# Performance work log

Hardware: AMD Instinct MI355X
Metric: run time of the kernel (lower is better)

The kernel has to match this reference:

```python
import jax, jax.numpy as jnp
import numpy as np
from jax import lax

NUM_CLASSES = 10
NUM_ITER = 3
CAP_DIM = 8       # primary capsule dim
OUT_CAP_DIM = 16  # digit capsule dim
NUM_MAP = 32      # 256 / 8
NUM_PRIM = 144    # 12*12


def squash(x, axis=-1):
    s2 = jnp.sum(x * x, axis=axis, keepdims=True)
    return (s2 / (1.0 + s2)) * x / jnp.sqrt(s2 + 1e-8)


def conv2d(x, w, b):
    y = lax.conv_general_dilated(x, w, (1, 1), 'VALID',
                                 dimension_numbers=('NCHW', 'OIHW', 'NCHW'))
    return y + b[None, :, None, None]


def setup_inputs() -> dict:
    key = jax.random.key(0)
    ks = jax.random.split(key, 13)
    B = 128
    return {
        'imgs': jax.random.uniform(ks[0], (B, 1, 28, 28), dtype=jnp.float32),
        'conv1_w': jax.random.normal(ks[1], (256, 1, 9, 9), jnp.float32) * 0.05,
        'conv1_b': jnp.zeros((256,), jnp.float32),
        'conv2_w': jax.random.normal(ks[2], (256, 256, 9, 9), jnp.float32) * 0.02,
        'conv2_b': jnp.zeros((256,), jnp.float32),
        # non-shared routing weights: [num_prim_map, num_prim_cap, num_classes, out_dim, in_dim]
        'W_digit': jax.random.normal(ks[3], (NUM_MAP, NUM_PRIM, NUM_CLASSES, OUT_CAP_DIM, CAP_DIM), jnp.float32),
        'dec_w1': jax.random.normal(ks[4], (OUT_CAP_DIM * NUM_CLASSES, 512), jnp.float32) * 0.05,
        'dec_b1': jnp.zeros((512,), jnp.float32),
        'dec_w2': jax.random.normal(ks[5], (512, 1024), jnp.float32) * 0.04,
        'dec_b2': jnp.zeros((1024,), jnp.float32),
        'dec_w3': jax.random.normal(ks[6], (1024, 784), jnp.float32) * 0.03,
        'dec_b3': jnp.zeros((784,), jnp.float32),
    }


def capsnet_fwd(imgs, conv1_w, conv1_b, conv2_w, conv2_b, W_digit,
                dec_w1, dec_b1, dec_w2, dec_b2, dec_w3, dec_b3):
    B = imgs.shape[0]
    # conv1 + relu: [B,256,20,20]
    x = jax.nn.relu(conv2d(imgs, conv1_w, conv1_b))
    # primary caps conv: [B,256,12,12]
    p = conv2d(x, conv2_w, conv2_b)
    # view [B, cap_dim, num_map, 12, 12] -> [B, num_map, 144, cap_dim]
    p = p.reshape(B, CAP_DIM, NUM_MAP, NUM_PRIM)
    p = jnp.transpose(p, (0, 2, 3, 1))
    u = squash(p, axis=-1)  # [B, 32, 144, 8]

    # u_hat[b,m,p,c,o] = W[m,p,c,o,i] * u[b,m,p,i]  (broadcast instead of repeat)
    u_hat = jnp.einsum('mpcoi,bmpi->bmpco', W_digit, u)
    u_hat = u_hat.reshape(B, NUM_MAP * NUM_PRIM, NUM_CLASSES, OUT_CAP_DIM)  # [B,4608,10,16]

    # dynamic routing
    b_ij = jnp.zeros((B, NUM_MAP * NUM_PRIM, NUM_CLASSES), u_hat.dtype)
    v = None
    for i in range(NUM_ITER):
        c_ij = jax.nn.softmax(b_ij, axis=1)                     # over input capsules
        s_j = jnp.einsum('bnc,bncd->bcd', c_ij, u_hat)          # [B,10,16]
        v = squash(s_j, axis=-1)
        if i != NUM_ITER - 1:
            b_ij = b_ij + jnp.einsum('bncd,bcd->bnc', u_hat, v)  # agreement

    # v: [B,10,16]
    v_length = jnp.sqrt(jnp.sum(v * v, axis=-1))                 # [B,10]
    y_pred = jnp.argmax(v_length, axis=1)
    y_pred_ohe = jax.nn.one_hot(y_pred, NUM_CLASSES, dtype=jnp.int32)

    masked = (v * y_pred_ohe.astype(v.dtype)[:, :, None]).reshape(B, -1)  # [B,160]
    h = jax.nn.relu(masked @ dec_w1 + dec_b1)
    h = jax.nn.relu(h @ dec_w2 + dec_b2)
    img_reconst = jax.nn.sigmoid(h @ dec_w3 + dec_b3)            # [B,784]
    return y_pred_ohe, img_reconst, v_length


def reference(imgs, conv1_w, conv1_b, conv2_w, conv2_b, W_digit,
              dec_w1, dec_b1, dec_w2, dec_b2, dec_w3, dec_b3):
    return capsnet_fwd(imgs, conv1_w, conv1_b, conv2_w, conv2_b, W_digit,
                       dec_w1, dec_b1, dec_w2, dec_b2, dec_w3, dec_b3)
```

## Files before the change

### kernel.cpp

```cpp
#include <hip/hip_runtime.h>
#include <cstdint>
#include <cstddef>

#define BB 128
#define NMAP 32
#define NPRIM 144
#define NCAP 4608
#define NCLS 10
#define ODIM 16
#define IDIM 8

#define WS_X1H  0
#define WS_X1L  6553600
#define WS_BH   13107200
#define WS_P    18415616
#define WS_U    23134208
#define WS_V    27852800
#define WS_H1   27873280
#define WS_H2   27938816
#define WS_CLS  28069888

#define OUT_REC  1280
#define OUT_LEN  101632

typedef __attribute__((ext_vector_type(8))) short short8;
typedef __attribute__((ext_vector_type(4))) float f32x4;

static __device__ __forceinline__ ushort f2bf(float f) {
    uint u = __float_as_uint(f);
    u = (u + 0x7FFFu + ((u >> 16) & 1u)) >> 16;
    return (ushort)u;
}
static __device__ __forceinline__ float bf2f(ushort h) {
    return __uint_as_float(((uint)h) << 16);
}

static __device__ __forceinline__ void gload16(const ushort* g, ushort* l) {
    __builtin_amdgcn_global_load_lds(
        (const __attribute__((address_space(1))) void*)g,
        (__attribute__((address_space(3))) void*)l, 16, 0, 0);
}


__global__ __launch_bounds__(256) void k_conv1(const float* __restrict__ img,
                                               const float* __restrict__ w,
                                               const float* __restrict__ bias,
                                               ushort* __restrict__ x1h,
                                               ushort* __restrict__ x1l) {
    __shared__ float simg[252];
    int bi = blockIdx.x;
    int y = bi % 20;
    int b = bi / 20;
    int oc = threadIdx.x;
    if (threadIdx.x < 252)
        simg[threadIdx.x] = img[(size_t)b * 784 + y * 28 + threadIdx.x];
    __syncthreads();

    float acc[20];
    float bv = bias[oc];
#pragma unroll
    for (int x = 0; x < 20; ++x) acc[x] = bv;
    const float* wp = w + oc * 81;
#pragma unroll
    for (int kh = 0; kh < 9; ++kh) {
        float r[28];
#pragma unroll
        for (int j = 0; j < 28; ++j) r[j] = simg[kh * 28 + j];
#pragma unroll
        for (int kw = 0; kw < 9; ++kw) {
            float wv = wp[kh * 9 + kw];
#pragma unroll
            for (int x = 0; x < 20; ++x)
                acc[x] = fmaf(wv, r[x + kw], acc[x]);
        }
    }
    size_t base = ((size_t)b * 400 + y * 20) * 256 + oc;
#pragma unroll
    for (int x = 0; x < 20; ++x) {
        float v = fmaxf(acc[x], 0.f);
        ushort h = f2bf(v);
        ushort lo = f2bf(v - bf2f(h));
        x1h[base + (size_t)x * 256] = h;
        x1l[base + (size_t)x * 256] = lo;
    }
}

__global__ __launch_bounds__(256) void k_prep_w2(const float* __restrict__ w2,
                                                 ushort* __restrict__ bpk) {
    int blk = blockIdx.x;
    int icc = blk >> 5, kq = (blk >> 3) & 3, ocg = blk & 7;
    int tid = threadIdx.x;
    int ocl = tid >> 3, ic8 = tid & 7;
    int oc = ocg * 32 + ocl;
    int ic = icc * 32 + kq * 8 + ic8;
    const float* src = w2 + ((size_t)oc * 256 + ic) * 81;
    size_t dbase = (size_t)icc * 16384 + (size_t)kq * 2048 + (size_t)oc * 8 + ic8;
#pragma unroll 9
    for (int t = 0; t < 81; ++t) {
        float v = src[t];
        ushort h = f2bf(v);
        ushort lo = f2bf(v - bf2f(h));
        bpk[(size_t)t * 131072 + dbase] = h;
        bpk[(size_t)t * 131072 + dbase + 8192] = lo;
    }
}

static __device__ __forceinline__ f32x4 mfma16(short8 a, short8 b, f32x4 c) {
    return __builtin_amdgcn_mfma_f32_16x16x32_bf16(a, b, c, 0, 0, 0);
}


template<int NMF>
static __device__ __forceinline__ void tap_body(
    f32x4 (&acc)[5][2], const ushort* A_lds, const ushort* Bc,
    const int* celloff, int tapoff, int bro0, int bro1) {
    short8 ah[5], al[5];
#pragma unroll
    for (int i = 0; i < NMF; ++i) {
        ah[i] = *(const short8*)(A_lds + tapoff + celloff[i]);
        al[i] = *(const short8*)(A_lds + 16000 + tapoff + celloff[i]);
    }
    short8 bh0 = *(const short8*)(Bc + bro0);
    short8 bh1 = *(const short8*)(Bc + bro1);
    short8 bl0 = *(const short8*)(Bc + 4096 + bro0);
    short8 bl1 = *(const short8*)(Bc + 4096 + bro1);
#pragma unroll
    for (int i = 0; i < NMF; ++i) {
        acc[i][0] = mfma16(ah[i], bh0, acc[i][0]);
        acc[i][1] = mfma16(ah[i], bh1, acc[i][1]);
    }
#pragma unroll
    for (int i = 0; i < NMF; ++i) {
        acc[i][0] = mfma16(ah[i], bl0, acc[i][0]);
        acc[i][1] = mfma16(ah[i], bl1, acc[i][1]);
    }
#pragma unroll
    for (int i = 0; i < NMF; ++i) {
        acc[i][0] = mfma16(al[i], bh0, acc[i][0]);
        acc[i][1] = mfma16(al[i], bh1, acc[i][1]);
    }
}

template<int MF0, int NMF>
static __device__ __forceinline__ void conv2s_epi(
    const f32x4 (&acc)[5][2], const float* __restrict__ bias,
    float* __restrict__ p, int b, int oc0, int nq, int r, int kq) {
#pragma unroll
    for (int j = 0; j < 2; ++j) {
        int oc = oc0 + (nq * 2 + j) * 16 + r;
        float bv = bias[oc];
#pragma unroll
        for (int i = 0; i < NMF; ++i) {
            int row = b * 144 + (MF0 + i) * 16 + kq * 4;
#pragma unroll
            for (int reg = 0; reg < 4; ++reg)
                p[(size_t)(row + reg) * 256 + oc] = acc[i][j][reg] + bv;
        }
    }
}

__global__ __launch_bounds__(512, 2) void k_conv2s(
    const ushort* __restrict__ x1h, const ushort* __restrict__ x1l,
    const ushort* __restrict__ bpk,
    const float* __restrict__ bias, float* __restrict__ p) {
    __shared__ __align__(16) ushort A_lds[32000];
    __shared__ __align__(16) ushort Bb[32768];

    const int tid = threadIdx.x;
    const int lane = tid & 63;
    const int wv = tid >> 6;
    const int mh = wv >> 2;
    const int nq = wv & 3;
    const int b  = blockIdx.x >> 1;
    const int nt = blockIdx.x & 1;
    const int oc0 = nt * 128;
    const int r = lane & 15, kq = lane >> 4;
    const int MF0r = mh ? 5 : 0;

    int celloff[5];
#pragma unroll
    for (int i = 0; i < 5; ++i) {
        int lm = (MF0r + i) * 16 + r;
        celloff[i] = ((lm / 12) * 20 + (lm % 12)) * 40 + kq * 8;
    }
    const int bro0 = kq * 1024 + ((nq * 2 + 0) * 16 + r) * 8;
    const int bro1 = kq * 1024 + ((nq * 2 + 1) * 16 + r) * 8;

    const int comp_w = wv >> 2, kq_w = wv & 3;
    const ushort* gB0 = bpk + comp_w * 8192 + kq_w * 2048 + oc0 * 8 + lane * 8;
    ushort* lB0 = Bb + comp_w * 4096 + kq_w * 1024;

    f32x4 acc[5][2];
#pragma unroll
    for (int i = 0; i < 5; ++i)
#pragma unroll
        for (int j = 0; j < 2; ++j)
            acc[i][j] = (f32x4){0.f, 0.f, 0.f, 0.f};

    for (int icc = 0; icc < 8; ++icc) {
        const size_t gicc = (size_t)icc * 16384;
#pragma unroll
        for (int rd = 0; rd < 7; ++rd) {
            int idx = rd * 512 + tid;
            if (idx < 3200) {
                int comp = (idx >= 1600) ? 1 : 0;
                int ci = idx - comp * 1600;
                int cell = ci >> 2, cc = ci & 3;
                const ushort* src = (comp ? x1l : x1h) +
                    ((size_t)b * 400 + cell) * 256 + icc * 32 + cc * 8;
                short8 val = *(const short8*)src;
                *(short8*)(A_lds + comp * 16000 + cell * 40 + cc * 8) = val;
            }
        }
        gload16(gB0 + gicc, lB0);
        gload16(gB0 + gicc + 512, lB0 + 512);
        gload16(gB0 + gicc + 131072, lB0 + 8192);
        gload16(gB0 + gicc + 131072 + 512, lB0 + 8192 + 512);
        __syncthreads();

#pragma unroll 1
        for (int ph = 0; ph < 39; ++ph) {
            const int T = ph * 2;
            {
                size_t g2 = (size_t)(T + 2) * 131072 + gicc;
                ushort* d2 = lB0 + ((T + 2) & 3) * 8192;
                gload16(gB0 + g2, d2);
                gload16(gB0 + g2 + 512, d2 + 512);
                size_t g3 = g2 + 131072;
                ushort* d3 = lB0 + ((T + 3) & 3) * 8192;
                gload16(gB0 + g3, d3);
                gload16(gB0 + g3 + 512, d3 + 512);
            }
            const int kh0 = T / 9, kw0 = T - kh0 * 9;
            const int tap0 = (kh0 * 20 + kw0) * 40;
            const int T1 = T + 1;
            const int kh1 = T1 / 9, kw1 = T1 - kh1 * 9;
            const int tap1 = (kh1 * 20 + kw1) * 40;
            const ushort* Bc0 = Bb + (T & 3) * 8192;
            const ushort* Bc1 = Bb + (T1 & 3) * 8192;
            if (mh == 0) {
                tap_body<5>(acc, A_lds, Bc0, celloff, tap0, bro0, bro1);
                tap_body<5>(acc, A_lds, Bc1, celloff, tap1, bro0, bro1);
            } else {
                tap_body<4>(acc, A_lds, Bc0, celloff, tap0, bro0, bro1);
                tap_body<4>(acc, A_lds, Bc1, celloff, tap1, bro0, bro1);
            }
            __syncthreads();
        }
        {
            size_t g80 = (size_t)80 * 131072 + gicc;
            gload16(gB0 + g80, lB0);
            gload16(gB0 + g80 + 512, lB0 + 512);
            if (mh == 0) {
                tap_body<5>(acc, A_lds, Bb + 2 * 8192, celloff, (8 * 20 + 6) * 40, bro0, bro1);
                tap_body<5>(acc, A_lds, Bb + 3 * 8192, celloff, (8 * 20 + 7) * 40, bro0, bro1);
            } else {
                tap_body<4>(acc, A_lds, Bb + 2 * 8192, celloff, (8 * 20 + 6) * 40, bro0, bro1);
                tap_body<4>(acc, A_lds, Bb + 3 * 8192, celloff, (8 * 20 + 7) * 40, bro0, bro1);
            }
            __syncthreads();
            if (mh == 0) tap_body<5>(acc, A_lds, Bb, celloff, (8 * 20 + 8) * 40, bro0, bro1);
            else         tap_body<4>(acc, A_lds, Bb, celloff, (8 * 20 + 8) * 40, bro0, bro1);
            __syncthreads();
        }
    }

    if (mh == 0) conv2s_epi<0, 5>(acc, bias, p, b, oc0, nq, r, kq);
    else         conv2s_epi<5, 4>(acc, bias, p, b, oc0, nq, r, kq);
}

__global__ __launch_bounds__(256) void k_squash(const float* __restrict__ p,
                                                float* __restrict__ u) {
    int id = blockIdx.x * 256 + threadIdx.x;
    int n = id % NCAP;
    int b = id / NCAP;
    int m = n / NPRIM, pos = n - m * NPRIM;
    const float* pp = p + ((size_t)b * 144 + pos) * 256 + m;
    float pv[8];
    float s2 = 0.f;
#pragma unroll
    for (int i = 0; i < 8; ++i) {
        pv[i] = pp[i * 32];
        s2 = fmaf(pv[i], pv[i], s2);
    }
    float f = (s2 / (1.f + s2)) / sqrtf(s2 + 1e-8f);
    float4 a = make_float4(f * pv[0], f * pv[1], f * pv[2], f * pv[3]);
    float4 c = make_float4(f * pv[4], f * pv[5], f * pv[6], f * pv[7]);
    float4* up = (float4*)(u + (size_t)id * 8);
    up[0] = a;
    up[1] = c;
}

__global__ __launch_bounds__(256) void k_prep_wt(const float* __restrict__ Wd,
                                                 float* __restrict__ Wt) {
    __shared__ float S[64][129];
    int c = blockIdx.x % NCLS;
    int nt = blockIdx.x / NCLS;
    int n0 = nt * 64;
    int tid = threadIdx.x;
#pragma unroll
    for (int rep = 0; rep < 32; ++rep) {
        int idx = rep * 256 + tid;
        int nl = idx >> 7, oi = idx & 127;
        S[nl][oi] = Wd[(size_t)(n0 + nl) * 1280 + c * 128 + oi];
    }
    __syncthreads();
#pragma unroll
    for (int rep = 0; rep < 32; ++rep) {
        int idx = rep * 256 + tid;
        int oi = idx >> 6, nl = idx & 63;
        Wt[((size_t)c * 128 + oi) * NCAP + n0 + nl] = S[nl][oi];
    }
}

__global__ __launch_bounds__(256) void k_route5(const float* __restrict__ u,
                                                const float* __restrict__ Wt,
                                                float* __restrict__ v_out) {
    __shared__ float part[4][2][17];
    __shared__ float sums[2][17];
    __shared__ float vsh[2][16];
    int c = blockIdx.x % NCLS;
    int bg = blockIdx.x / NCLS;
    int b0 = bg * 2;
    int tid = threadIdx.x;
    int lane = tid & 63, wvi = tid >> 6;
    const float* WtC = Wt + (size_t)c * 128 * NCAP;

    float bij[18][2];
#pragma unroll
    for (int j = 0; j < 18; ++j) { bij[j][0] = 0.f; bij[j][1] = 0.f; }

    for (int iter = 0; iter < 3; ++iter) {
        float sZ[2] = {0.f, 0.f};
        float sS[2][16];
#pragma unroll
        for (int o = 0; o < 16; ++o) { sS[0][o] = 0.f; sS[1][o] = 0.f; }

        for (int j = 0; j < 18; ++j) {
            int n = j * 256 + tid;
            const float4* up0 = (const float4*)(u + ((size_t)b0 * NCAP + n) * 8);
            const float4* up1 = (const float4*)(u + ((size_t)(b0 + 1) * NCAP + n) * 8);
            float4 a0 = up0[0], a1 = up0[1];
            float4 c0 = up1[0], c1 = up1[1];
            float u0[8] = {a0.x, a0.y, a0.z, a0.w, a1.x, a1.y, a1.z, a1.w};
            float u1[8] = {c0.x, c0.y, c0.z, c0.w, c1.x, c1.y, c1.z, c1.w};
            float uh[2][16];
#pragma unroll
            for (int o = 0; o < 16; ++o) {
                float s0 = 0.f, s1 = 0.f;
#pragma unroll
                for (int i = 0; i < 8; ++i) {
                    float w = WtC[(size_t)(o * 8 + i) * NCAP + n];
                    s0 = fmaf(w, u0[i], s0);
                    s1 = fmaf(w, u1[i], s1);
                }
                uh[0][o] = s0;
                uh[1][o] = s1;
            }
#pragma unroll
            for (int bb = 0; bb < 2; ++bb) {
                float e;
                if (iter == 0) {
                    e = 1.f;
                } else {
                    float agr = 0.f;
#pragma unroll
                    for (int o = 0; o < 16; ++o) agr = fmaf(uh[bb][o], vsh[bb][o], agr);
                    bij[j][bb] += agr;
                    e = __expf(bij[j][bb]);
                }
                sZ[bb] += e;
#pragma unroll
                for (int o = 0; o < 16; ++o) sS[bb][o] = fmaf(e, uh[bb][o], sS[bb][o]);
            }
        }

#pragma unroll
        for (int bb = 0; bb < 2; ++bb) {
            float z = sZ[bb];
#pragma unroll
            for (int d = 32; d >= 1; d >>= 1) z += __shfl_xor(z, d, 64);
            if (lane == 0) part[wvi][bb][0] = z;
#pragma unroll
            for (int o = 0; o < 16; ++o) {
                float s = sS[bb][o];
#pragma unroll
                for (int d = 32; d >= 1; d >>= 1) s += __shfl_xor(s, d, 64);
                if (lane == 0) part[wvi][bb][1 + o] = s;
            }
        }
        __syncthreads();
        if (tid < 34) {
            int bb = tid / 17, k = tid % 17;
            float s = 0.f;
#pragma unroll
            for (int w4 = 0; w4 < 4; ++w4) s += part[w4][bb][k];
            sums[bb][k] = s;
        }
        __syncthreads();
        if (tid < 2) {
            float Z = sums[tid][0];
            float s[16];
            float s2 = 0.f;
#pragma unroll
            for (int o = 0; o < 16; ++o) {
                s[o] = sums[tid][1 + o] / Z;
                s2 = fmaf(s[o], s[o], s2);
            }
            float f = (s2 / (1.f + s2)) / sqrtf(s2 + 1e-8f);
#pragma unroll
            for (int o = 0; o < 16; ++o) vsh[tid][o] = f * s[o];
        }
        __syncthreads();
    }
    if (tid < 32) {
        int bb = tid >> 4, o = tid & 15;
        v_out[((size_t)(b0 + bb) * NCLS + c) * 16 + o] = vsh[bb][o];
    }
}

__global__ __launch_bounds__(64) void k_head(const float* __restrict__ v,
                                             float* __restrict__ out,
                                             int* __restrict__ cls_ws) {
    __shared__ float len2[NCLS];
    __shared__ int cls_sh;
    int b = blockIdx.x, tid = threadIdx.x;
    if (tid < NCLS) {
        float s2 = 0.f;
#pragma unroll
        for (int o = 0; o < 16; ++o) {
            float t = v[((size_t)b * NCLS + tid) * 16 + o];
            s2 = fmaf(t, t, s2);
        }
        len2[tid] = s2;
        out[OUT_LEN + b * NCLS + tid] = sqrtf(s2);
    }
    __syncthreads();
    if (tid == 0) {
        int best = 0;
        float bv = len2[0];
        for (int c2 = 1; c2 < NCLS; ++c2)
            if (len2[c2] > bv) { bv = len2[c2]; best = c2; }
        cls_sh = best;
        cls_ws[b] = best;
    }
    __syncthreads();
    if (tid < NCLS) out[b * NCLS + tid] = (tid == cls_sh) ? 1.0f : 0.0f;
}

__global__ __launch_bounds__(256) void k_dec1(const float* __restrict__ v,
                                              const int* __restrict__ cls_ws,
                                              const float* __restrict__ w1,
                                              const float* __restrict__ b1,
                                              float* __restrict__ h1) {
    int id = blockIdx.x * 256 + threadIdx.x;
    int j = id % 512, b = id / 512;
    int cls = cls_ws[b];
    const float* vp = v + ((size_t)b * NCLS + cls) * 16;
    float acc = b1[j];
#pragma unroll
    for (int o = 0; o < 16; ++o)
        acc = fmaf(vp[o], w1[(size_t)(cls * 16 + o) * 512 + j], acc);
    h1[id] = fmaxf(acc, 0.f);
}

__global__ __launch_bounds__(256) void k_dec2(const float* __restrict__ h1,
                                              const float* __restrict__ w2,
                                              const float* __restrict__ b2,
                                              float* __restrict__ h2) {
    __shared__ float hs[512];
    int bi = blockIdx.x;
    int jc = bi % 4;
    int b = bi / 4;
    int tid = threadIdx.x;
    hs[tid] = h1[b * 512 + tid];
    hs[tid + 256] = h1[b * 512 + tid + 256];
    __syncthreads();
    int j = jc * 256 + tid;
    float acc = b2[j];
#pragma unroll 8
    for (int k = 0; k < 512; ++k)
        acc = fmaf(hs[k], w2[(size_t)k * 1024 + j], acc);
    h2[b * 1024 + j] = fmaxf(acc, 0.f);
}

__global__ __launch_bounds__(256) void k_dec3(const float* __restrict__ h2,
                                              const float* __restrict__ w3,
                                              const float* __restrict__ b3,
                                              float* __restrict__ out) {
    __shared__ float hs[1024];
    int bi = blockIdx.x;
    int jc = bi % 4;
    int b = bi / 4;
    int tid = threadIdx.x;
#pragma unroll
    for (int t = 0; t < 4; ++t) hs[tid + t * 256] = h2[b * 1024 + tid + t * 256];
    __syncthreads();
    int j = jc * 256 + tid;
    if (j < 784) {
        float acc = b3[j];
#pragma unroll 8
        for (int k = 0; k < 1024; ++k)
            acc = fmaf(hs[k], w3[(size_t)k * 784 + j], acc);
        out[OUT_REC + b * 784 + j] = 1.f / (1.f + __expf(-acc));
    }
}

extern "C" void kernel_launch(void* const* d_in, const int* in_sizes, int n_in,
                              void* d_out, int out_size, void* d_ws, size_t ws_size,
                              hipStream_t stream) {
    const float* imgs = (const float*)d_in[0];
    const float* c1w  = (const float*)d_in[1];
    const float* c1b  = (const float*)d_in[2];
    const float* c2w  = (const float*)d_in[3];
    const float* c2b  = (const float*)d_in[4];
    const float* Wd   = (const float*)d_in[5];
    const float* dw1  = (const float*)d_in[6];
    const float* db1  = (const float*)d_in[7];
    const float* dw2  = (const float*)d_in[8];
    const float* db2  = (const float*)d_in[9];
    const float* dw3  = (const float*)d_in[10];
    const float* db3  = (const float*)d_in[11];

    float* out = (float*)d_out;
    float* ws  = (float*)d_ws;
    ushort* x1h = (ushort*)(ws + WS_X1H);
    ushort* x1l = (ushort*)(ws + WS_X1L);
    ushort* bpk = (ushort*)(ws + WS_BH);
    float* p    = ws + WS_P;
    float* u    = ws + WS_U;
    float* v    = ws + WS_V;
    float* h1   = ws + WS_H1;
    float* h2   = ws + WS_H2;
    int*   cls  = (int*)(ws + WS_CLS);
    float* wt32 = ws + WS_X1H;

    k_conv1<<<BB * 20, 256, 0, stream>>>(imgs, c1w, c1b, x1h, x1l);
    k_prep_w2<<<256, 256, 0, stream>>>(c2w, bpk);
    k_conv2s<<<BB * 2, 512, 0, stream>>>(x1h, x1l, bpk, c2b, p);
    k_squash<<<BB * NCAP / 256, 256, 0, stream>>>(p, u);
    k_prep_wt<<<720, 256, 0, stream>>>(Wd, wt32);
    k_route5<<<(BB / 2) * NCLS, 256, 0, stream>>>(u, wt32, v);
    k_head<<<BB, 64, 0, stream>>>(v, out, cls);
    k_dec1<<<BB * 512 / 256, 256, 0, stream>>>(v, cls, dw1, db1, h1);
    k_dec2<<<BB * 4, 256, 0, stream>>>(h1, dw2, db2, h2);
    k_dec3<<<BB * 4, 256, 0, stream>>>(h2, dw3, db3, out);
}
```

Measured before the change: 1.179 ms.

## Split conv2 taps across wave pairs with 2x4 tiles and LDS reduction

Re-partitions the eight waves of the primary-caps conv kernel. Previously each wave computed both taps of a phase for a 5x2 MFMA tile. Now each wave handles one of the two taps with a 5x4 tile (M-half by N-half), and the two tap-partial accumulators are summed through LDS before the epilogue. This raises B-fragment reuse per A load and halves A LDS reads per MFMA. The cost is twice the accumulator registers, which may hurt occupancy at 2 blocks per CU, plus an extra LDS reduction and idle waves on the odd final tap.

```diff
diff --git a/kernel.cpp b/kernel.cpp
--- a/kernel.cpp
+++ b/kernel.cpp
@@ -111,43 +111,44 @@
 
 
 template<int NMF>
-static __device__ __forceinline__ void tap_body(
-    f32x4 (&acc)[5][2], const ushort* A_lds, const ushort* Bc,
-    const int* celloff, int tapoff, int bro0, int bro1) {
-    short8 ah[5], al[5];
+static __device__ __forceinline__ void tap_body32(
+    f32x4 (&acc)[5][4], const ushort* A_lds, const ushort* Bc,
+    const int* celloff, int tapoff, const int* bro) {
+    short8 ah[5], al[5], bh[4], bl[4];
 #pragma unroll
     for (int i = 0; i < NMF; ++i) {
         ah[i] = *(const short8*)(A_lds + tapoff + celloff[i]);
         al[i] = *(const short8*)(A_lds + 16000 + tapoff + celloff[i]);
     }
-    short8 bh0 = *(const short8*)(Bc + bro0);
-    short8 bh1 = *(const short8*)(Bc + bro1);
-    short8 bl0 = *(const short8*)(Bc + 4096 + bro0);
-    short8 bl1 = *(const short8*)(Bc + 4096 + bro1);
-#pragma unroll
-    for (int i = 0; i < NMF; ++i) {
-        acc[i][0] = mfma16(ah[i], bh0, acc[i][0]);
-        acc[i][1] = mfma16(ah[i], bh1, acc[i][1]);
-    }
-#pragma unroll
-    for (int i = 0; i < NMF; ++i) {
-        acc[i][0] = mfma16(ah[i], bl0, acc[i][0]);
-        acc[i][1] = mfma16(ah[i], bl1, acc[i][1]);
-    }
-#pragma unroll
-    for (int i = 0; i < NMF; ++i) {
-        acc[i][0] = mfma16(al[i], bh0, acc[i][0]);
-        acc[i][1] = mfma16(al[i], bh1, acc[i][1]);
-    }
+#pragma unroll
+    for (int j = 0; j < 4; ++j) {
+        bh[j] = *(const short8*)(Bc + bro[j]);
+        bl[j] = *(const short8*)(Bc + 4096 + bro[j]);
+    }
+#pragma unroll
+    for (int i = 0; i < NMF; ++i)
+#pragma unroll
+        for (int j = 0; j < 4; ++j)
+            acc[i][j] = mfma16(ah[i], bh[j], acc[i][j]);
+#pragma unroll
+    for (int i = 0; i < NMF; ++i)
+#pragma unroll
+        for (int j = 0; j < 4; ++j)
+            acc[i][j] = mfma16(ah[i], bl[j], acc[i][j]);
+#pragma unroll
+    for (int i = 0; i < NMF; ++i)
+#pragma unroll
+        for (int j = 0; j < 4; ++j)
+            acc[i][j] = mfma16(al[i], bh[j], acc[i][j]);
 }
 
 template<int MF0, int NMF>
-static __device__ __forceinline__ void conv2s_epi(
-    const f32x4 (&acc)[5][2], const float* __restrict__ bias,
-    float* __restrict__ p, int b, int oc0, int nq, int r, int kq) {
-#pragma unroll
-    for (int j = 0; j < 2; ++j) {
-        int oc = oc0 + (nq * 2 + j) * 16 + r;
+static __device__ __forceinline__ void conv2s_epi4(
+    const f32x4 (&acc)[5][4], const float* __restrict__ bias,
+    float* __restrict__ p, int b, int oc0, int nh, int r, int kq) {
+#pragma unroll
+    for (int j = 0; j < 4; ++j) {
+        int oc = oc0 + (nh * 4 + j) * 16 + r;
         float bv = bias[oc];
 #pragma unroll
         for (int i = 0; i < NMF; ++i) {
@@ -169,8 +170,9 @@
     const int tid = threadIdx.x;
     const int lane = tid & 63;
     const int wv = tid >> 6;
-    const int mh = wv >> 2;
-    const int nq = wv & 3;
+    const int tp = wv >> 2;
+    const int mh = (wv >> 1) & 1;
+    const int nh = wv & 1;
     const int b  = blockIdx.x >> 1;
     const int nt = blockIdx.x & 1;
     const int oc0 = nt * 128;
@@ -183,18 +185,20 @@
         int lm = (MF0r + i) * 16 + r;
         celloff[i] = ((lm / 12) * 20 + (lm % 12)) * 40 + kq * 8;
     }
-    const int bro0 = kq * 1024 + ((nq * 2 + 0) * 16 + r) * 8;
-    const int bro1 = kq * 1024 + ((nq * 2 + 1) * 16 + r) * 8;
+    int bro[4];
+#pragma unroll
+    for (int j = 0; j < 4; ++j)
+        bro[j] = kq * 1024 + ((nh * 4 + j) * 16 + r) * 8;
 
     const int comp_w = wv >> 2, kq_w = wv & 3;
     const ushort* gB0 = bpk + comp_w * 8192 + kq_w * 2048 + oc0 * 8 + lane * 8;
     ushort* lB0 = Bb + comp_w * 4096 + kq_w * 1024;
 
-    f32x4 acc[5][2];
+    f32x4 acc[5][4];
 #pragma unroll
     for (int i = 0; i < 5; ++i)
 #pragma unroll
-        for (int j = 0; j < 2; ++j)
+        for (int j = 0; j < 4; ++j)
             acc[i][j] = (f32x4){0.f, 0.f, 0.f, 0.f};
 
     for (int icc = 0; icc < 8; ++icc) {
@@ -231,42 +235,59 @@
                 gload16(gB0 + g3, d3);
                 gload16(gB0 + g3 + 512, d3 + 512);
             }
-            const int kh0 = T / 9, kw0 = T - kh0 * 9;
-            const int tap0 = (kh0 * 20 + kw0) * 40;
-            const int T1 = T + 1;
-            const int kh1 = T1 / 9, kw1 = T1 - kh1 * 9;
-            const int tap1 = (kh1 * 20 + kw1) * 40;
-            const ushort* Bc0 = Bb + (T & 3) * 8192;
-            const ushort* Bc1 = Bb + (T1 & 3) * 8192;
-            if (mh == 0) {
-                tap_body<5>(acc, A_lds, Bc0, celloff, tap0, bro0, bro1);
-                tap_body<5>(acc, A_lds, Bc1, celloff, tap1, bro0, bro1);
-            } else {
-                tap_body<4>(acc, A_lds, Bc0, celloff, tap0, bro0, bro1);
-                tap_body<4>(acc, A_lds, Bc1, celloff, tap1, bro0, bro1);
-            }
+            const int tn = T + tp;
+            const int kh = tn / 9, kw = tn - kh * 9;
+            const int tapoff = (kh * 20 + kw) * 40;
+            const ushort* Bc = Bb + (tn & 3) * 8192;
+            if (mh == 0) tap_body32<5>(acc, A_lds, Bc, celloff, tapoff, bro);
+            else         tap_body32<4>(acc, A_lds, Bc, celloff, tapoff, bro);
             __syncthreads();
         }
         {
             size_t g80 = (size_t)80 * 131072 + gicc;
             gload16(gB0 + g80, lB0);
             gload16(gB0 + g80 + 512, lB0 + 512);
-            if (mh == 0) {
-                tap_body<5>(acc, A_lds, Bb + 2 * 8192, celloff, (8 * 20 + 6) * 40, bro0, bro1);
-                tap_body<5>(acc, A_lds, Bb + 3 * 8192, celloff, (8 * 20 + 7) * 40, bro0, bro1);
-            } else {
-                tap_body<4>(acc, A_lds, Bb + 2 * 8192, celloff, (8 * 20 + 6) * 40, bro0, bro1);
-                tap_body<4>(acc, A_lds, Bb + 3 * 8192, celloff, (8 * 20 + 7) * 40, bro0, bro1);
-            }
+            const int tn = 78 + tp;
+            const int tapoff = (8 * 20 + (6 + tp)) * 40;
+            const ushort* Bc = Bb + (tn & 3) * 8192;
+            if (mh == 0) tap_body32<5>(acc, A_lds, Bc, celloff, tapoff, bro);
+            else         tap_body32<4>(acc, A_lds, Bc, celloff, tapoff, bro);
             __syncthreads();
-            if (mh == 0) tap_body<5>(acc, A_lds, Bb, celloff, (8 * 20 + 8) * 40, bro0, bro1);
-            else         tap_body<4>(acc, A_lds, Bb, celloff, (8 * 20 + 8) * 40, bro0, bro1);
+            if (tp == 0) {
+                if (mh == 0) tap_body32<5>(acc, A_lds, Bb, celloff, (8 * 20 + 8) * 40, bro);
+                else         tap_body32<4>(acc, A_lds, Bb, celloff, (8 * 20 + 8) * 40, bro);
+            }
             __syncthreads();
         }
     }
 
-    if (mh == 0) conv2s_epi<0, 5>(acc, bias, p, b, oc0, nq, r, kq);
-    else         conv2s_epi<5, 4>(acc, bias, p, b, oc0, nq, r, kq);
+    const int wvq = mh * 2 + nh;
+    float* red = (wvq < 2) ? ((float*)A_lds + wvq * 5120)
+                           : ((float*)Bb + (wvq - 2) * 5120);
+    const int NMFr = mh ? 4 : 5;
+    if (tp == 1) {
+#pragma unroll
+        for (int i = 0; i < 5; ++i) {
+            if (i < NMFr)
+#pragma unroll
+                for (int j = 0; j < 4; ++j)
+                    *(f32x4*)(red + ((i * 4 + j) * 64 + lane) * 4) = acc[i][j];
+        }
+    }
+    __syncthreads();
+    if (tp == 0) {
+#pragma unroll
+        for (int i = 0; i < 5; ++i) {
+            if (i < NMFr)
+#pragma unroll
+                for (int j = 0; j < 4; ++j) {
+                    f32x4 o = *(const f32x4*)(red + ((i * 4 + j) * 64 + lane) * 4);
+                    acc[i][j] += o;
+                }
+        }
+        if (mh == 0) conv2s_epi4<0, 5>(acc, bias, p, b, oc0, nh, r, kq);
+        else         conv2s_epi4<5, 4>(acc, bias, p, b, oc0, nh, r, kq);
+    }
 }
 
 __global__ __launch_bounds__(256) void k_squash(const float* __restrict__ p,
```

Result: no change. 1.184 ms (+0.5%).
